# Kernel tuning notes

Measured on AMD Instinct MI355X. Metric: run time of the kernel, lower is better.

The kernel has to match this reference:

```python
import jax, jax.numpy as jnp
import numpy as np

N_NODES = 100000
N_EDGES = 1600000
F_IN, NH1, NH2, NH3, N_CLS = 128, 64, 18, 9, 10
KS = [8, 6, 4, 4]
BN_EPS = 1e-5


def setup_inputs() -> dict:
    key = jax.random.key(0)
    ks = jax.random.split(key, 32)
    inp = {
        "x": jax.random.normal(ks[0], (N_NODES, F_IN), dtype=jnp.float32),
        "edge_index": jax.random.randint(ks[1], (2, N_EDGES), 0, N_NODES, dtype=jnp.int32),
    }
    dims = [(F_IN, NH1), (NH1, NH2), (NH2, NH3), (NH3, N_CLS)]
    for i, ((din, dout), K) in enumerate(zip(dims, KS), start=1):
        scale = 1.0 / np.sqrt(din * K)
        inp[f"W{i}"] = jax.random.normal(ks[2 * i], (K, din, dout), dtype=jnp.float32) * scale
        inp[f"b{i}"] = jnp.zeros((dout,), dtype=jnp.float32)
    for i, d in enumerate([NH1, NH2, NH3], start=1):
        inp[f"bn{i}_g"] = jnp.ones((d,), dtype=jnp.float32)
        inp[f"bn{i}_b"] = jnp.zeros((d,), dtype=jnp.float32)
        inp[f"bn{i}_m"] = jnp.zeros((d,), dtype=jnp.float32)
        inp[f"bn{i}_v"] = jnp.ones((d,), dtype=jnp.float32)
    return inp


def _cheb_conv(x, W, b, src, dst, w_norm, n_nodes):
    # PyG ChebConv with lambda_max=2: L_hat = -D^{-1/2} A D^{-1/2}
    def prop(t):  # L_hat @ t via edge scatter
        return jax.ops.segment_sum(w_norm[:, None] * t[src], dst, num_segments=n_nodes)

    K = W.shape[0]
    Tx0 = x
    out = Tx0 @ W[0]
    Tx1 = prop(Tx0)
    out = out + Tx1 @ W[1]
    for k in range(2, K):
        Tx2 = 2.0 * prop(Tx1) - Tx0
        out = out + Tx2 @ W[k]
        Tx0, Tx1 = Tx1, Tx2
    return out + b


def _bn_eval(x, g, b, m, v):
    return (x - m) * (g * jax.lax.rsqrt(v + BN_EPS)) + b


def reference(x, edge_index, W1, b1, W2, b2, W3, b3, W4, b4,
              bn1_g, bn1_b, bn1_m, bn1_v,
              bn2_g, bn2_b, bn2_m, bn2_v,
              bn3_g, bn3_b, bn3_m, bn3_v):
    n = x.shape[0]
    src, dst = edge_index[0], edge_index[1]
    ones = jnp.ones((src.shape[0],), dtype=x.dtype)
    deg = jax.ops.segment_sum(ones, dst, num_segments=n)
    dinv = jnp.where(deg > 0, jax.lax.rsqrt(jnp.maximum(deg, 1.0)), 0.0)
    w_norm = -dinv[src] * dinv[dst]

    h = jax.nn.relu(_bn_eval(_cheb_conv(x, W1, b1, src, dst, w_norm, n), bn1_g, bn1_b, bn1_m, bn1_v))
    h = jax.nn.relu(_bn_eval(_cheb_conv(h, W2, b2, src, dst, w_norm, n), bn2_g, bn2_b, bn2_m, bn2_v))
    h = jax.nn.relu(_bn_eval(_cheb_conv(h, W3, b3, src, dst, w_norm, n), bn3_g, bn3_b, bn3_m, bn3_v))
    return _cheb_conv(h, W4, b4, src, dst, w_norm, n)
```

## Files before the change

kernel.cpp:

```cpp
#include <hip/hip_runtime.h>

#define NN 100000
#define NE 1600000
#define BN_EPS 1e-5f

typedef _Float16 half1;
typedef _Float16 half4 __attribute__((ext_vector_type(4)));
typedef _Float16 h8 __attribute__((ext_vector_type(8)));
typedef float f4 __attribute__((ext_vector_type(4)));

static inline int divup(int a, int b) { return (a + b - 1) / b; }


__global__ void hist_kernel(const int* __restrict__ dst, int* __restrict__ deg, int e) {
    int i = blockIdx.x * blockDim.x + threadIdx.x;
    if (i < e) atomicAdd(&deg[dst[i]], 1);
}

__global__ void blksum_kernel(const int* __restrict__ deg, int* __restrict__ blk, int n) {
    __shared__ int red[256];
    int t = threadIdx.x;
    int base = blockIdx.x * 1024 + t * 4;
    int s = 0;
#pragma unroll
    for (int i = 0; i < 4; ++i) {
        int idx = base + i;
        if (idx < n) s += deg[idx];
    }
    red[t] = s;
    __syncthreads();
    for (int off = 128; off > 0; off >>= 1) {
        if (t < off) red[t] += red[t + off];
        __syncthreads();
    }
    if (t == 0) blk[blockIdx.x] = red[0];
}

__global__ void blkscan_kernel(int* __restrict__ blk, int nb, int* __restrict__ row_ptr, int n) {
    __shared__ int sh[256];
    int t = threadIdx.x;
    int v = (t < nb) ? blk[t] : 0;
    sh[t] = v;
    __syncthreads();
    for (int off = 1; off < 256; off <<= 1) {
        int u = (t >= off) ? sh[t - off] : 0;
        __syncthreads();
        sh[t] += u;
        __syncthreads();
    }
    if (t < nb) blk[t] = (t == 0) ? 0 : sh[t - 1];
    if (t == nb - 1) row_ptr[n] = sh[t];
}

__global__ void emit_kernel(const int* __restrict__ deg, const int* __restrict__ blk,
                            int* __restrict__ row_ptr, int n) {
    __shared__ int red[256];
    int t = threadIdx.x;
    int base = blockIdx.x * 1024 + t * 4;
    int d[4];
    int s = 0;
#pragma unroll
    for (int i = 0; i < 4; ++i) {
        int idx = base + i;
        d[i] = (idx < n) ? deg[idx] : 0;
        s += d[i];
    }
    red[t] = s;
    __syncthreads();
    for (int off = 1; off < 256; off <<= 1) {
        int u = (t >= off) ? red[t - off] : 0;
        __syncthreads();
        red[t] += u;
        __syncthreads();
    }
    int run = blk[blockIdx.x] + ((t == 0) ? 0 : red[t - 1]);
#pragma unroll
    for (int i = 0; i < 4; ++i) {
        int idx = base + i;
        if (idx < n) { row_ptr[idx] = run; run += d[i]; }
    }
}

__global__ void dinv_kernel(const int* __restrict__ deg, float* __restrict__ dinv, int n) {
    int i = blockIdx.x * blockDim.x + threadIdx.x;
    if (i < n) {
        int d = deg[i];
        dinv[i] = (d > 0) ? rsqrtf((float)d) : 0.f;
    }
}

__global__ void scatter_kernel(const int* __restrict__ src, const int* __restrict__ dst,
                               const int* __restrict__ row_ptr, int* __restrict__ cursor,
                               const float* __restrict__ dinv,
                               int2* __restrict__ cw, int e) {
    int i = blockIdx.x * blockDim.x + threadIdx.x;
    if (i >= e) return;
    int s = src[i], d = dst[i];
    int pos = row_ptr[d] + atomicAdd(&cursor[d], 1);
    cw[pos] = make_int2(s, __float_as_int(-dinv[s] * dinv[d]));
}


__global__ void cvtx_kernel(const float4* __restrict__ X, half4* __restrict__ Xh, int tot4) {
    int i = blockIdx.x * blockDim.x + threadIdx.x;
    if (i >= tot4) return;
    float4 v = X[i];
    half4 h;
    h.x = (half1)v.x; h.y = (half1)v.y; h.z = (half1)v.z; h.w = (half1)v.w;
    Xh[i] = h;
}

__global__ void transw_kernel(const float* __restrict__ W, half1* __restrict__ Wt) {
    int i = blockIdx.x * blockDim.x + threadIdx.x;
    if (i >= 512 * 128) return;
    int kd = i >> 9;
    int og = i & 511;
    int k = og >> 6, o = og & 63;
    Wt[(size_t)og * 128 + kd] = (half1)W[((size_t)k * 128 + kd) * 64 + o];
}

__global__ void padw_kernel(const float* __restrict__ src, float* __restrict__ dst,
                            int K, int dins, int douts, int dind, int doutd) {
    int i = blockIdx.x * blockDim.x + threadIdx.x;
    int tot = K * dind * doutd;
    if (i >= tot) return;
    int o = i % doutd;
    int r = i / doutd;
    int dd = r % dind;
    int k = r / dind;
    dst[i] = (dd < dins && o < douts) ? src[((size_t)k * dins + dd) * douts + o] : 0.f;
}

__global__ void proph_kernel(const half4* __restrict__ feat, const half4* __restrict__ sub,
                             const half4* __restrict__ add, half4* __restrict__ outh,
                             f4* __restrict__ outf,
                             const int* __restrict__ row_ptr, const int2* __restrict__ cw,
                             int n, int dim4, float scale, int has_sub,
                             int bnrelu, int used,
                             const float* __restrict__ bn_g, const float* __restrict__ bn_b,
                             const float* __restrict__ bn_m, const float* __restrict__ bn_v) {
    int idx = blockIdx.x * blockDim.x + threadIdx.x;
    if (idx >= n * dim4) return;
    int nd = idx / dim4;
    int f = idx - nd * dim4;
    int e0 = row_ptr[nd], e1 = row_ptr[nd + 1];
    f4 a0 = {0.f, 0.f, 0.f, 0.f}, a1 = a0, a2 = a0, a3 = a0;
    int e = e0;
    for (; e + 4 <= e1; e += 4) {
        int2 q0 = cw[e], q1 = cw[e + 1], q2 = cw[e + 2], q3 = cw[e + 3];
        f4 v0 = __builtin_convertvector(feat[(size_t)q0.x * dim4 + f], f4);
        f4 v1 = __builtin_convertvector(feat[(size_t)q1.x * dim4 + f], f4);
        f4 v2 = __builtin_convertvector(feat[(size_t)q2.x * dim4 + f], f4);
        f4 v3 = __builtin_convertvector(feat[(size_t)q3.x * dim4 + f], f4);
        a0 += __int_as_float(q0.y) * v0;
        a1 += __int_as_float(q1.y) * v1;
        a2 += __int_as_float(q2.y) * v2;
        a3 += __int_as_float(q3.y) * v3;
    }
    for (; e < e1; ++e) {
        int2 q = cw[e];
        f4 v = __builtin_convertvector(feat[(size_t)q.x * dim4 + f], f4);
        a0 += __int_as_float(q.y) * v;
    }
    f4 r = ((a0 + a1) + (a2 + a3)) * scale;
    if (has_sub) r -= __builtin_convertvector(sub[idx], f4);
    r += __builtin_convertvector(add[idx], f4);
    if (bnrelu) {
#pragma unroll
        for (int c = 0; c < 4; ++c) {
            int o = f * 4 + c;
            if (o < used) {
                float sc = bn_g[o] * rsqrtf(bn_v[o] + BN_EPS);
                r[c] = fmaxf(fmaf(r[c] - bn_m[o], sc, bn_b[o]), 0.f);
            } else r[c] = 0.f;
        }
    }
    if (outf) {
        outf[idx] = r;
    } else {
        half4 h;
        h.x = (half1)r.x; h.y = (half1)r.y; h.z = (half1)r.z; h.w = (half1)r.w;
        outh[idx] = h;
    }
}

__global__ void propl_kernel(const half4* __restrict__ feat, const half4* __restrict__ sub,
                             const half4* __restrict__ add, float* __restrict__ out,
                             const int* __restrict__ row_ptr, const int2* __restrict__ cw,
                             int n) {
    int idx = blockIdx.x * blockDim.x + threadIdx.x;
    if (idx >= n * 3) return;
    int nd = idx / 3;
    int f = idx - nd * 3;
    int e0 = row_ptr[nd], e1 = row_ptr[nd + 1];
    f4 a0 = {0.f, 0.f, 0.f, 0.f}, a1 = a0, a2 = a0, a3 = a0;
    int e = e0;
    for (; e + 4 <= e1; e += 4) {
        int2 q0 = cw[e], q1 = cw[e + 1], q2 = cw[e + 2], q3 = cw[e + 3];
        a0 += __int_as_float(q0.y) * __builtin_convertvector(feat[(size_t)q0.x * 3 + f], f4);
        a1 += __int_as_float(q1.y) * __builtin_convertvector(feat[(size_t)q1.x * 3 + f], f4);
        a2 += __int_as_float(q2.y) * __builtin_convertvector(feat[(size_t)q2.x * 3 + f], f4);
        a3 += __int_as_float(q3.y) * __builtin_convertvector(feat[(size_t)q3.x * 3 + f], f4);
    }
    for (; e < e1; ++e) {
        int2 q = cw[e];
        a0 += __int_as_float(q.y) * __builtin_convertvector(feat[(size_t)q.x * 3 + f], f4);
    }
    f4 r = (a0 + a1) + (a2 + a3);
    r -= __builtin_convertvector(sub[idx], f4);
    r += __builtin_convertvector(add[idx], f4);
    int o = f * 4;
    float* orow = out + (size_t)nd * 10;
    if (o + 0 < 10) orow[o + 0] = r.x;
    if (o + 1 < 10) orow[o + 1] = r.y;
    if (o + 2 < 10) orow[o + 2] = r.z;
    if (o + 3 < 10) orow[o + 3] = r.w;
}

__global__ __launch_bounds__(256) void gemm_mfma_kernel(
        const half1* __restrict__ Xh, const half1* __restrict__ Wt,
        const float* __restrict__ bias, half1* __restrict__ CB, int n) {
    int lane = threadIdx.x & 63;
    int wave = threadIdx.x >> 6;
    int m16 = lane & 15;
    int quad = lane >> 4;
    int ks = blockIdx.y * 4 + wave;
    int ntile = blockIdx.x * 64;

    f4 acc[4][4];
#pragma unroll
    for (int nt = 0; nt < 4; ++nt)
#pragma unroll
        for (int i = 0; i < 4; ++i) acc[nt][i] = (f4){0.f, 0.f, 0.f, 0.f};

#pragma unroll
    for (int kc = 0; kc < 4; ++kc) {
        int koff = kc * 32 + quad * 8;
        h8 a[4];
#pragma unroll
        for (int i = 0; i < 4; ++i)
            a[i] = *(const h8*)(Wt + (size_t)(ks * 64 + i * 16 + m16) * 128 + koff);
        h8 b[4];
#pragma unroll
        for (int nt = 0; nt < 4; ++nt) {
            int node = min(ntile + nt * 16 + m16, n - 1);
            b[nt] = *(const h8*)(Xh + (size_t)node * 128 + koff);
        }
#pragma unroll
        for (int nt = 0; nt < 4; ++nt)
#pragma unroll
            for (int i = 0; i < 4; ++i)
                acc[nt][i] = __builtin_amdgcn_mfma_f32_16x16x32_f16(a[i], b[nt], acc[nt][i], 0, 0, 0);
    }

#pragma unroll
    for (int nt = 0; nt < 4; ++nt) {
        int node = ntile + nt * 16 + m16;
        if (node < n) {
#pragma unroll
            for (int i = 0; i < 4; ++i) {
                int ob = i * 16 + quad * 4;
                f4 v = acc[nt][i];
                if (ks == 0) {
                    const f4 b4 = *(const f4*)(bias + ob);
                    v += b4;
                }
                half4 h;
                h.x = (half1)v[0]; h.y = (half1)v[1]; h.z = (half1)v[2]; h.w = (half1)v[3];
                *(half4*)(CB + ((size_t)ks * n + node) * 64 + ob) = h;
            }
        }
    }
}

template <int KK, int DIN4, int NACC>
__global__ void gemm_smallw_kernel(const float* __restrict__ X, const float* __restrict__ Wp,
                                   const float* __restrict__ bias, int dout,
                                   half4* __restrict__ CB, int n) {
    int lane = threadIdx.x & 63;
    int k = __builtin_amdgcn_readfirstlane((int)(threadIdx.x >> 6));
    int node0 = blockIdx.x * 64 + lane;
    int node = min(node0, n - 1);
    f4 acc[NACC];
#pragma unroll
    for (int i = 0; i < NACC; ++i) {
        f4 v = {0.f, 0.f, 0.f, 0.f};
        if (k == 0 && bias) {
#pragma unroll
            for (int c = 0; c < 4; ++c) {
                int o = i * 4 + c;
                v[c] = (o < dout) ? bias[o] : 0.f;
            }
        }
        acc[i] = v;
    }
    const f4* Xr = (const f4*)(X + (size_t)node * (DIN4 * 4));
    const f4* Wk = (const f4*)(Wp + (size_t)k * (DIN4 * 4) * (NACC * 4));
    for (int d4 = 0; d4 < DIN4; ++d4) {
        f4 xv = Xr[d4];
#pragma unroll
        for (int j = 0; j < 4; ++j) {
            float xs = xv[j];
#pragma unroll
            for (int i = 0; i < NACC; ++i)
                acc[i] += xs * Wk[(d4 * 4 + j) * NACC + i];
        }
    }
    if (node0 < n) {
        size_t base = ((size_t)k * n + node) * NACC;
#pragma unroll
        for (int i = 0; i < NACC; ++i) {
            half4 h;
            h.x = (half1)acc[i].x; h.y = (half1)acc[i].y;
            h.z = (half1)acc[i].z; h.w = (half1)acc[i].w;
            CB[base + i] = h;
        }
    }
}


extern "C" void kernel_launch(void* const* d_in, const int* in_sizes, int n_in,
                              void* d_out, int out_size, void* d_ws, size_t ws_size,
                              hipStream_t stream) {
    const float* x  = (const float*)d_in[0];
    const int*   ei = (const int*)d_in[1];
    const float* Wl[4] = {(const float*)d_in[2], (const float*)d_in[4],
                          (const float*)d_in[6], (const float*)d_in[8]};
    const float* bl[4] = {(const float*)d_in[3], (const float*)d_in[5],
                          (const float*)d_in[7], (const float*)d_in[9]};
    const float* bn[3][4];
    for (int l = 0; l < 3; ++l)
        for (int j = 0; j < 4; ++j)
            bn[l][j] = (const float*)d_in[10 + 4 * l + j];

    char* ws = (char*)d_ws;
    size_t off = 0;
    auto alloc = [&](size_t bytes) -> void* {
        void* p = (void*)(ws + off);
        off = (off + bytes + 255) & ~(size_t)255;
        return p;
    };
    int*   deg     = (int*)alloc(NN * 4);
    int*   row_ptr = (int*)alloc((NN + 1) * 4);
    int*   cursor  = (int*)alloc(NN * 4);
    int*   blks    = (int*)alloc(128 * 4);
    float* dinv    = (float*)alloc(NN * 4);
    int2*  cw      = (int2*)alloc((size_t)NE * 8);
    half1* CB1h    = (half1*)alloc((size_t)8 * NN * 64 * 2);
    half1* CBsh    = (half1*)alloc((size_t)6 * NN * 20 * 2);
    half1* S0      = (half1*)alloc((size_t)NN * 64 * 2);
    half1* S1      = (half1*)alloc((size_t)NN * 64 * 2);
    half1* S2      = (half1*)alloc((size_t)NN * 64 * 2);
    float* H1f     = (float*)alloc((size_t)NN * 64 * 4);
    float* H2f     = (float*)alloc((size_t)NN * 20 * 4);
    float* H3f     = (float*)alloc((size_t)NN * 12 * 4);
    float* Wp2     = (float*)alloc((size_t)6 * 64 * 20 * 4);
    float* Wp3     = (float*)alloc((size_t)4 * 20 * 12 * 4);
    float* Wp4     = (float*)alloc((size_t)4 * 12 * 12 * 4);
    half1* Xh      = (half1*)alloc((size_t)NN * 128 * 2);
    half1* Wt1     = (half1*)alloc((size_t)512 * 128 * 2);

    const int* srcp = ei;
    const int* dstp = ei + NE;
    const int nscan = divup(NN, 1024);
    const int NB = divup(NN, 64);

    hipMemsetAsync(deg, 0, NN * 4, stream);
    hipMemsetAsync(cursor, 0, NN * 4, stream);
    hist_kernel<<<divup(NE, 256), 256, 0, stream>>>(dstp, deg, NE);
    blksum_kernel<<<nscan, 256, 0, stream>>>(deg, blks, NN);
    blkscan_kernel<<<1, 256, 0, stream>>>(blks, nscan, row_ptr, NN);
    emit_kernel<<<nscan, 256, 0, stream>>>(deg, blks, row_ptr, NN);
    dinv_kernel<<<divup(NN, 256), 256, 0, stream>>>(deg, dinv, NN);
    scatter_kernel<<<divup(NE, 256), 256, 0, stream>>>(srcp, dstp, row_ptr, cursor, dinv, cw, NE);

    cvtx_kernel<<<divup(NN * 32, 256), 256, 0, stream>>>((const float4*)x, (half4*)Xh, NN * 32);
    transw_kernel<<<divup(512 * 128, 256), 256, 0, stream>>>(Wl[0], Wt1);
    padw_kernel<<<divup(6 * 64 * 20, 256), 256, 0, stream>>>(Wl[1], Wp2, 6, 64, 18, 64, 20);
    padw_kernel<<<divup(4 * 20 * 12, 256), 256, 0, stream>>>(Wl[2], Wp3, 4, 18, 9, 20, 12);
    padw_kernel<<<divup(4 * 12 * 12, 256), 256, 0, stream>>>(Wl[3], Wp4, 4, 9, 10, 12, 12);

    auto prop = [&](const half1* feat, const half1* sub, const half1* add,
                    half1* outh, float* outf, int dim4, float scale,
                    int bnrelu, int used, const float* g, const float* bb,
                    const float* m, const float* v) {
        proph_kernel<<<divup(NN * dim4, 256), 256, 0, stream>>>(
            (const half4*)feat, (const half4*)sub, (const half4*)add,
            (half4*)outh, (f4*)outf, row_ptr, cw, NN, dim4, scale,
            sub != nullptr, bnrelu, used, g, bb, m, v);
    };

    gemm_mfma_kernel<<<dim3(NB, 2), 256, 0, stream>>>(Xh, Wt1, bl[0], CB1h, NN);
    {
        auto C = [&](int k) { return (const half1*)(CB1h + (size_t)k * NN * 64); };
        prop(C(7), nullptr, C(6), S0, nullptr, 16, 2.f, 0, 64, 0, 0, 0, 0);
        prop(S0, C(7), C(5), S1, nullptr, 16, 2.f, 0, 64, 0, 0, 0, 0);
        prop(S1, S0, C(4), S2, nullptr, 16, 2.f, 0, 64, 0, 0, 0, 0);
        prop(S2, S1, C(3), S0, nullptr, 16, 2.f, 0, 64, 0, 0, 0, 0);
        prop(S0, S2, C(2), S1, nullptr, 16, 2.f, 0, 64, 0, 0, 0, 0);
        prop(S1, S0, C(1), S2, nullptr, 16, 2.f, 0, 64, 0, 0, 0, 0);
        prop(S2, S1, C(0), nullptr, H1f, 16, 1.f, 1, 64,
             bn[0][0], bn[0][1], bn[0][2], bn[0][3]);
    }

    gemm_smallw_kernel<6, 16, 5><<<NB, 384, 0, stream>>>(H1f, Wp2, bl[1], 18,
                                                         (half4*)CBsh, NN);
    {
        auto C = [&](int k) { return (const half1*)(CBsh + (size_t)k * NN * 20); };
        prop(C(5), nullptr, C(4), S0, nullptr, 5, 2.f, 0, 18, 0, 0, 0, 0);
        prop(S0, C(5), C(3), S1, nullptr, 5, 2.f, 0, 18, 0, 0, 0, 0);
        prop(S1, S0, C(2), S2, nullptr, 5, 2.f, 0, 18, 0, 0, 0, 0);
        prop(S2, S1, C(1), S0, nullptr, 5, 2.f, 0, 18, 0, 0, 0, 0);
        prop(S0, S2, C(0), nullptr, H2f, 5, 1.f, 1, 18,
             bn[1][0], bn[1][1], bn[1][2], bn[1][3]);
    }

    gemm_smallw_kernel<4, 5, 3><<<NB, 256, 0, stream>>>(H2f, Wp3, bl[2], 9,
                                                        (half4*)CBsh, NN);
    {
        auto C = [&](int k) { return (const half1*)(CBsh + (size_t)k * NN * 12); };
        prop(C(3), nullptr, C(2), S0, nullptr, 3, 2.f, 0, 9, 0, 0, 0, 0);
        prop(S0, C(3), C(1), S1, nullptr, 3, 2.f, 0, 9, 0, 0, 0, 0);
        prop(S1, S0, C(0), nullptr, H3f, 3, 1.f, 1, 9,
             bn[2][0], bn[2][1], bn[2][2], bn[2][3]);
    }

    gemm_smallw_kernel<4, 3, 3><<<NB, 256, 0, stream>>>(H3f, Wp4, bl[3], 10,
                                                        (half4*)CBsh, NN);
    {
        auto C = [&](int k) { return (const half1*)(CBsh + (size_t)k * NN * 12); };
        prop(C(3), nullptr, C(2), S0, nullptr, 3, 2.f, 0, 10, 0, 0, 0, 0);
        prop(S0, C(3), C(1), S1, nullptr, 3, 2.f, 0, 10, 0, 0, 0, 0);
        propl_kernel<<<divup(NN * 3, 256), 256, 0, stream>>>(
            (const half4*)S1, (const half4*)S0, (const half4*)CBsh,
            (float*)d_out, row_ptr, cw, NN);
    }
}
```

Before: 914.5 us.

## Two-pass bucketed CSR scatter and 8-wide half gathers for layer-1 propagation

New measurement: 1.223 ms. +33.7%, slower.

```diff
diff --git a/kernel.cpp b/kernel.cpp
--- a/kernel.cpp
+++ b/kernel.cpp
@@ -3,11 +3,14 @@
 #define NN 100000
 #define NE 1600000
 #define BN_EPS 1e-5f
+#define BSHIFT 7
+#define NBUCK ((NN + 127) >> 7)
 
 typedef _Float16 half1;
 typedef _Float16 half4 __attribute__((ext_vector_type(4)));
 typedef _Float16 h8 __attribute__((ext_vector_type(8)));
 typedef float f4 __attribute__((ext_vector_type(4)));
+typedef float f8 __attribute__((ext_vector_type(8)));
 
 static inline int divup(int a, int b) { return (a + b - 1) / b; }
 
@@ -89,15 +92,25 @@
     }
 }
 
-__global__ void scatter_kernel(const int* __restrict__ src, const int* __restrict__ dst,
-                               const int* __restrict__ row_ptr, int* __restrict__ cursor,
-                               const float* __restrict__ dinv,
-                               int2* __restrict__ cw, int e) {
+__global__ void binA_kernel(const int* __restrict__ src, const int* __restrict__ dst,
+                            const int* __restrict__ row_ptr, int* __restrict__ bcur,
+                            int2* __restrict__ tmp, int e) {
     int i = blockIdx.x * blockDim.x + threadIdx.x;
     if (i >= e) return;
     int s = src[i], d = dst[i];
-    int pos = row_ptr[d] + atomicAdd(&cursor[d], 1);
-    cw[pos] = make_int2(s, __float_as_int(-dinv[s] * dinv[d]));
+    int b = d >> BSHIFT;
+    int pos = row_ptr[b << BSHIFT] + atomicAdd(&bcur[b], 1);
+    tmp[pos] = make_int2(s, d);
+}
+
+__global__ void binB_kernel(const int2* __restrict__ tmp, const int* __restrict__ row_ptr,
+                            int* __restrict__ cursor, const float* __restrict__ dinv,
+                            int2* __restrict__ cw, int e) {
+    int i = blockIdx.x * blockDim.x + threadIdx.x;
+    if (i >= e) return;
+    int2 sd = tmp[i];
+    int pos = row_ptr[sd.y] + atomicAdd(&cursor[sd.y], 1);
+    cw[pos] = make_int2(sd.x, __float_as_int(-dinv[sd.x] * dinv[sd.y]));
 }
 
 
@@ -129,6 +142,53 @@
     int dd = r % dind;
     int k = r / dind;
     dst[i] = (dd < dins && o < douts) ? src[((size_t)k * dins + dd) * douts + o] : 0.f;
+}
+
+__global__ void proph8_kernel(const h8* __restrict__ feat, const h8* __restrict__ sub,
+                              const h8* __restrict__ add, h8* __restrict__ outh,
+                              f8* __restrict__ outf,
+                              const int* __restrict__ row_ptr, const int2* __restrict__ cw,
+                              int n, float scale, int has_sub, int bnrelu,
+                              const float* __restrict__ bn_g, const float* __restrict__ bn_b,
+                              const float* __restrict__ bn_m, const float* __restrict__ bn_v) {
+    int idx = blockIdx.x * blockDim.x + threadIdx.x;
+    if (idx >= n * 8) return;
+    int nd = idx >> 3;
+    int f = idx & 7;
+    int e0 = row_ptr[nd], e1 = row_ptr[nd + 1];
+    f8 a0 = {0.f, 0.f, 0.f, 0.f, 0.f, 0.f, 0.f, 0.f}, a1 = a0, a2 = a0, a3 = a0;
+    int e = e0;
+    for (; e + 4 <= e1; e += 4) {
+        int2 q0 = cw[e], q1 = cw[e + 1], q2 = cw[e + 2], q3 = cw[e + 3];
+        f8 v0 = __builtin_convertvector(feat[(size_t)q0.x * 8 + f], f8);
+        f8 v1 = __builtin_convertvector(feat[(size_t)q1.x * 8 + f], f8);
+        f8 v2 = __builtin_convertvector(feat[(size_t)q2.x * 8 + f], f8);
+        f8 v3 = __builtin_convertvector(feat[(size_t)q3.x * 8 + f], f8);
+        a0 += __int_as_float(q0.y) * v0;
+        a1 += __int_as_float(q1.y) * v1;
+        a2 += __int_as_float(q2.y) * v2;
+        a3 += __int_as_float(q3.y) * v3;
+    }
+    for (; e < e1; ++e) {
+        int2 q = cw[e];
+        a0 += __int_as_float(q.y) * __builtin_convertvector(feat[(size_t)q.x * 8 + f], f8);
+    }
+    f8 r = ((a0 + a1) + (a2 + a3)) * scale;
+    if (has_sub) r -= __builtin_convertvector(sub[idx], f8);
+    r += __builtin_convertvector(add[idx], f8);
+    if (bnrelu) {
+#pragma unroll
+        for (int c = 0; c < 8; ++c) {
+            int o = f * 8 + c;
+            float sc = bn_g[o] * rsqrtf(bn_v[o] + BN_EPS);
+            r[c] = fmaxf(fmaf(r[c] - bn_m[o], sc, bn_b[o]), 0.f);
+        }
+    }
+    if (outf) {
+        outf[idx] = r;
+    } else {
+        outh[idx] = __builtin_convertvector(r, h8);
+    }
 }
 
 __global__ void proph_kernel(const half4* __restrict__ feat, const half4* __restrict__ sub,
@@ -159,8 +219,7 @@
     }
     for (; e < e1; ++e) {
         int2 q = cw[e];
-        f4 v = __builtin_convertvector(feat[(size_t)q.x * dim4 + f], f4);
-        a0 += __int_as_float(q.y) * v;
+        a0 += __int_as_float(q.y) * __builtin_convertvector(feat[(size_t)q.x * dim4 + f], f4);
     }
     f4 r = ((a0 + a1) + (a2 + a3)) * scale;
     if (has_sub) r -= __builtin_convertvector(sub[idx], f4);
@@ -343,9 +402,11 @@
     int*   deg     = (int*)alloc(NN * 4);
     int*   row_ptr = (int*)alloc((NN + 1) * 4);
     int*   cursor  = (int*)alloc(NN * 4);
+    int*   bcur    = (int*)alloc(NBUCK * 4);
     int*   blks    = (int*)alloc(128 * 4);
     float* dinv    = (float*)alloc(NN * 4);
     int2*  cw      = (int2*)alloc((size_t)NE * 8);
+    int2*  tmp     = (int2*)alloc((size_t)NE * 8);
     half1* CB1h    = (half1*)alloc((size_t)8 * NN * 64 * 2);
     half1* CBsh    = (half1*)alloc((size_t)6 * NN * 20 * 2);
     half1* S0      = (half1*)alloc((size_t)NN * 64 * 2);
@@ -367,12 +428,14 @@
 
     hipMemsetAsync(deg, 0, NN * 4, stream);
     hipMemsetAsync(cursor, 0, NN * 4, stream);
+    hipMemsetAsync(bcur, 0, NBUCK * 4, stream);
     hist_kernel<<<divup(NE, 256), 256, 0, stream>>>(dstp, deg, NE);
     blksum_kernel<<<nscan, 256, 0, stream>>>(deg, blks, NN);
     blkscan_kernel<<<1, 256, 0, stream>>>(blks, nscan, row_ptr, NN);
     emit_kernel<<<nscan, 256, 0, stream>>>(deg, blks, row_ptr, NN);
     dinv_kernel<<<divup(NN, 256), 256, 0, stream>>>(deg, dinv, NN);
-    scatter_kernel<<<divup(NE, 256), 256, 0, stream>>>(srcp, dstp, row_ptr, cursor, dinv, cw, NE);
+    binA_kernel<<<divup(NE, 256), 256, 0, stream>>>(srcp, dstp, row_ptr, bcur, tmp, NE);
+    binB_kernel<<<divup(NE, 256), 256, 0, stream>>>(tmp, row_ptr, cursor, dinv, cw, NE);
 
     cvtx_kernel<<<divup(NN * 32, 256), 256, 0, stream>>>((const float4*)x, (half4*)Xh, NN * 32);
     transw_kernel<<<divup(512 * 128, 256), 256, 0, stream>>>(Wl[0], Wt1);
@@ -380,6 +443,14 @@
     padw_kernel<<<divup(4 * 20 * 12, 256), 256, 0, stream>>>(Wl[2], Wp3, 4, 18, 9, 20, 12);
     padw_kernel<<<divup(4 * 12 * 12, 256), 256, 0, stream>>>(Wl[3], Wp4, 4, 9, 10, 12, 12);
 
+    auto prop1 = [&](const half1* feat, const half1* sub, const half1* add,
+                     half1* outh, float* outf, float scale, int bnrelu,
+                     const float* g, const float* bb, const float* m, const float* v) {
+        proph8_kernel<<<divup(NN * 8, 256), 256, 0, stream>>>(
+            (const h8*)feat, (const h8*)sub, (const h8*)add,
+            (h8*)outh, (f8*)outf, row_ptr, cw, NN, scale,
+            sub != nullptr, bnrelu, g, bb, m, v);
+    };
     auto prop = [&](const half1* feat, const half1* sub, const half1* add,
                     half1* outh, float* outf, int dim4, float scale,
                     int bnrelu, int used, const float* g, const float* bb,
@@ -393,14 +464,14 @@
     gemm_mfma_kernel<<<dim3(NB, 2), 256, 0, stream>>>(Xh, Wt1, bl[0], CB1h, NN);
     {
         auto C = [&](int k) { return (const half1*)(CB1h + (size_t)k * NN * 64); };
-        prop(C(7), nullptr, C(6), S0, nullptr, 16, 2.f, 0, 64, 0, 0, 0, 0);
-        prop(S0, C(7), C(5), S1, nullptr, 16, 2.f, 0, 64, 0, 0, 0, 0);
-        prop(S1, S0, C(4), S2, nullptr, 16, 2.f, 0, 64, 0, 0, 0, 0);
-        prop(S2, S1, C(3), S0, nullptr, 16, 2.f, 0, 64, 0, 0, 0, 0);
-        prop(S0, S2, C(2), S1, nullptr, 16, 2.f, 0, 64, 0, 0, 0, 0);
-        prop(S1, S0, C(1), S2, nullptr, 16, 2.f, 0, 64, 0, 0, 0, 0);
-        prop(S2, S1, C(0), nullptr, H1f, 16, 1.f, 1, 64,
-             bn[0][0], bn[0][1], bn[0][2], bn[0][3]);
+        prop1(C(7), nullptr, C(6), S0, nullptr, 2.f, 0, 0, 0, 0, 0);
+        prop1(S0, C(7), C(5), S1, nullptr, 2.f, 0, 0, 0, 0, 0);
+        prop1(S1, S0, C(4), S2, nullptr, 2.f, 0, 0, 0, 0, 0);
+        prop1(S2, S1, C(3), S0, nullptr, 2.f, 0, 0, 0, 0, 0);
+        prop1(S0, S2, C(2), S1, nullptr, 2.f, 0, 0, 0, 0, 0);
+        prop1(S1, S0, C(1), S2, nullptr, 2.f, 0, 0, 0, 0, 0);
+        prop1(S2, S1, C(0), nullptr, H1f, 1.f, 1,
+              bn[0][0], bn[0][1], bn[0][2], bn[0][3]);
     }
 
     gemm_smallw_kernel<6, 16, 5><<<NB, 384, 0, stream>>>(H1f, Wp2, bl[1], 18,
```
